# Performance work log

Hardware: AMD Instinct MI355X
Metric: run time of the kernel (lower is better)

Reference implementation:

```python
import jax, jax.numpy as jnp
import numpy as np

B, S, L, F, CD, NH, E, HID = 4, 1024, 256, 512, 768, 8, 8, 2048


def _xavier(k, shape):
    std = float(np.sqrt(1.0 / (shape[-2] + shape[-1])))
    return jax.random.normal(k, shape, dtype=jnp.float32) * std


def setup_inputs() -> dict:
    key = jax.random.key(0)
    ks = iter(jax.random.split(key, 64))
    nk = lambda: next(ks)
    inp = {}
    inp['x_r'] = jax.random.normal(nk(), (B, S, F), jnp.float32)
    inp['x_i'] = jax.random.normal(nk(), (B, S, F), jnp.float32)
    inp['ctx_r'] = jax.random.normal(nk(), (B, L, CD), jnp.float32)
    inp['ctx_i'] = jax.random.normal(nk(), (B, L, CD), jnp.float32)
    inp['ln1_g'] = jnp.ones((F,), jnp.float32)
    inp['ln2_g'] = jnp.ones((F,), jnp.float32)
    inp['ln3_g'] = jnp.ones((F,), jnp.float32)
    for pref, shp in [('sa_q', (F, F)), ('sa_k', (F, F)), ('sa_v', (F, F)), ('sa_o', (F, F)),
                      ('ca_q', (F, F)), ('ca_k', (CD, F)), ('ca_v', (CD, F)), ('ca_o', (F, F))]:
        inp[pref + 'Wr'] = _xavier(nk(), shp)
        inp[pref + 'Wi'] = _xavier(nk(), shp)
        inp[pref + 'br'] = jnp.zeros((F,), jnp.float32)
        inp[pref + 'bi'] = jnp.zeros((F,), jnp.float32)
    inp['moe_W1r'] = _xavier(nk(), (E, F, HID))
    inp['moe_W1i'] = _xavier(nk(), (E, F, HID))
    inp['moe_b1r'] = jnp.zeros((E, HID), jnp.float32)
    inp['moe_b1i'] = jnp.zeros((E, HID), jnp.float32)
    inp['moe_mb'] = jnp.zeros((E, HID), jnp.float32)  # modReLU bias
    inp['moe_W2r'] = _xavier(nk(), (E, HID, F))
    inp['moe_W2i'] = _xavier(nk(), (E, HID, F))
    inp['moe_b2r'] = jnp.zeros((E, F), jnp.float32)
    inp['moe_b2i'] = jnp.zeros((E, F), jnp.float32)
    return inp


def _clin(xr, xi, Wr, Wi, br, bi):
    # (xr + i xi) @ (Wr + i Wi) + (br + i bi)
    return xr @ Wr - xi @ Wi + br, xr @ Wi + xi @ Wr + bi


def _cln(xr, xi, g, eps=1e-6):
    amp = jnp.sqrt(xr * xr + xi * xi + eps)
    s = g * (amp / (jnp.mean(amp, axis=-1, keepdims=True) + eps)) / (amp + eps)
    return xr * s, xi * s


def _modrelu(xr, xi, b, eps=1e-10):
    amp = jnp.sqrt(xr * xr + xi * xi + eps)
    s = jax.nn.relu(amp + b) / (amp + eps)
    return xr * s, xi * s


def _cattn(xr, xi, cr, ci, qWr, qWi, qbr, qbi, kWr, kWi, kbr, kbi,
           vWr, vWi, vbr, vbi, oWr, oWi, obr, obi, nh):
    qr, qi = _clin(xr, xi, qWr, qWi, qbr, qbi)
    kr, ki = _clin(cr, ci, kWr, kWi, kbr, kbi)
    vr, vi = _clin(cr, ci, vWr, vWi, vbr, vbi)
    Bt, Sq, Ft = qr.shape
    Sk = kr.shape[1]
    d = Ft // nh
    sp = lambda t: t.reshape(Bt, t.shape[1], nh, d).transpose(0, 2, 1, 3)  # b n s d
    Qr, Qi, Kr, Ki, Vr, Vi = sp(qr), sp(qi), sp(kr), sp(ki), sp(vr), sp(vi)
    scale = 1.0 / float(d) ** 0.5
    scores = (jnp.einsum('bnqd,bnkd->bnqk', Qr, Kr)
              + jnp.einsum('bnqd,bnkd->bnqk', Qi, Ki)) * scale
    w = jax.nn.softmax(scores, axis=-1)
    mix = lambda t: jnp.einsum('bnqk,bnkd->bnqd', w, t).transpose(0, 2, 1, 3).reshape(Bt, Sq, Ft)
    return _clin(mix(Vr), mix(Vi), oWr, oWi, obr, obi)


def reference(x_r, x_i, ctx_r, ctx_i, ln1_g, ln2_g, ln3_g,
              sa_qWr, sa_qWi, sa_qbr, sa_qbi, sa_kWr, sa_kWi, sa_kbr, sa_kbi,
              sa_vWr, sa_vWi, sa_vbr, sa_vbi, sa_oWr, sa_oWi, sa_obr, sa_obi,
              ca_qWr, ca_qWi, ca_qbr, ca_qbi, ca_kWr, ca_kWi, ca_kbr, ca_kbi,
              ca_vWr, ca_vWi, ca_vbr, ca_vbi, ca_oWr, ca_oWi, ca_obr, ca_obi,
              moe_W1r, moe_W1i, moe_b1r, moe_b1i, moe_mb,
              moe_W2r, moe_W2i, moe_b2r, moe_b2i):
    # self-attention block
    hr, hi = _cln(x_r, x_i, ln1_g)
    ar, ai = _cattn(hr, hi, hr, hi, sa_qWr, sa_qWi, sa_qbr, sa_qbi,
                    sa_kWr, sa_kWi, sa_kbr, sa_kbi, sa_vWr, sa_vWi, sa_vbr, sa_vbi,
                    sa_oWr, sa_oWi, sa_obr, sa_obi, NH)
    xr, xi = x_r + ar, x_i + ai
    # cross-attention block
    hr, hi = _cln(xr, xi, ln2_g)
    ar, ai = _cattn(hr, hi, ctx_r, ctx_i, ca_qWr, ca_qWi, ca_qbr, ca_qbi,
                    ca_kWr, ca_kWi, ca_kbr, ca_kbi, ca_vWr, ca_vWi, ca_vbr, ca_vbi,
                    ca_oWr, ca_oWi, ca_obr, ca_obi, NH)
    xr, xi = xr + ar, xi + ai
    # phase-routed MoE block
    hr, hi = _cln(xr, xi, ln3_g)
    phase = jnp.arctan2(hi, hr)
    token_phase = jnp.arctan2(jnp.mean(jnp.sin(phase), axis=-1),
                              jnp.mean(jnp.cos(phase), axis=-1))
    idx = jnp.clip(jnp.floor((token_phase + jnp.pi) / (2.0 * jnp.pi) * E).astype(jnp.int32), 0, E - 1)
    acc_r = jnp.zeros_like(hr)
    acc_i = jnp.zeros_like(hi)
    for e in range(E):  # dense-compute-then-mask, faithful to source
        ur, ui = _clin(hr, hi, moe_W1r[e], moe_W1i[e], moe_b1r[e], moe_b1i[e])
        ur, ui = _modrelu(ur, ui, moe_mb[e])
        yr, yi = _clin(ur, ui, moe_W2r[e], moe_W2i[e], moe_b2r[e], moe_b2i[e])
        m = (idx == e).astype(hr.dtype)[..., None]
        acc_r = acc_r + yr * m
        acc_i = acc_i + yi * m
    xr, xi = xr + acc_r, xi + acc_i
    return jnp.stack([xr, xi])  # [2, B, S, F] real/imag
```

## Files before the change

kernel.cpp:

```cpp
#include <hip/hip_runtime.h>
#include <hip/hip_bf16.h>
#include <math.h>


#define NTOK 4096
#define FF   512
#define CDIM 768
#define NEXP 8
#define HID  2048
#define TMAX128 40
#define NPAD128 (TMAX128 * 128)

typedef __hip_bfloat16 bf16;
typedef short bf16x8 __attribute__((ext_vector_type(8)));
typedef float f32x4  __attribute__((ext_vector_type(4)));

struct Ptr6 { const float* p[6]; };
struct WPackAll {
    const float* sR[8]; const float* sI[8];
    bf16* dR[8]; bf16* dI[8];
    int kdiv[8];
};

__device__ __forceinline__ short f2bf(float x) {
// ... 129 lines not shown
    for (int j = 0; j < 8; j++) {
        float a = sR[(long)(kb + j) * N + n];
        bf16 ah = __float2bfloat16(a);
        dR[dbase + j] = lo ? __float2bfloat16(a - __bfloat162float(ah)) : ah;
        float b = sI[(long)(kb + j) * N + n];
        bf16 bh = __float2bfloat16(b);
        dI[dbase + j] = lo ? __float2bfloat16(b - __bfloat162float(bh)) : bh;
    }
}

__global__ __launch_bounds__(256)
void convW_packed(const float* __restrict__ sR, const float* __restrict__ sI,
                  bf16* __restrict__ dR, bf16* __restrict__ dI,
                  int N, long estride)
{
    int g = blockIdx.x * 256 + threadIdx.x;
    int nt = g >> 6, l = g & 63;
    int kc = blockIdx.y;
    int e  = blockIdx.z;
    const float* srcR = sR + (long)e * estride;
    const float* srcI = sI + (long)e * estride;
    bf16* dstR = dR + (long)e * estride;
    bf16* dstI = dI + (long)e * estride;
    int kb = kc * 32 + (l >> 4) * 8;
    int n  = nt * 16 + (l & 15);
    long dbase = ((long)kc * (N >> 4) + nt) * 512 + l * 8;
#pragma unroll
    for (int j = 0; j < 8; j++) {
        dstR[dbase + j] = __float2bfloat16(srcR[(long)(kb + j) * N + n]);
        dstI[dbase + j] = __float2bfloat16(srcI[(long)(kb + j) * N + n]);
    }
}

template<bool X3, bool EXPERT, bool GATHER, bool MODRELU, bool OUTBF16>
__global__ __launch_bounds__(256, 2)
void cgemm128(const bf16* __restrict__ Ar, const bf16* __restrict__ Ai,
              int lda, int Kreal,
              const bf16* __restrict__ Wr0, const bf16* __restrict__ Wi0,
              long wz, long westride, int ntTot, int kdiv,
              Ptr6 bias, int bstride, const float* __restrict__ mb,
              void* __restrict__ Cr0, void* __restrict__ Ci0, long cz,
              int ldc, int Kp, int bandM,
              const int* __restrict__ order, const int* __restrict__ tileExpert)
{
    __shared__ short sA[16384];
    __shared__ short sW[16384];
    int tm, tn, z;
    if (bandM > 0) {
        int L = blockIdx.x;
        int xcd = L & 7, idx = L >> 3;
        tm = xcd * bandM + idx % bandM;
        tn = idx / bandM;
        z = 0;
    } else {
        tm = blockIdx.x; tn = blockIdx.y; z = blockIdx.z;
    }
    const bf16* Wr = Wr0 + (long)z * wz;
    const bf16* Wi = Wi0 + (long)z * wz;
    const float* br = bias.p[2 * z];
    const float* bi = bias.p[2 * z + 1];
    void* Crv = (char*)Cr0 + (long)z * cz;
    void* Civ = (char*)Ci0 + (long)z * cz;
    if (EXPERT) {
        int e = tileExpert[tm];
        if (e < 0) return;
        Wr += (long)e * westride;  Wi += (long)e * westride;
        br += (long)e * bstride;   bi += (long)e * bstride;
        if (MODRELU) mb += (long)e * bstride;
    }
    int t = threadIdx.x;
    int l = t & 63, w = t >> 6;
    int riS = w >> 1, kcS = w & 1;
    const bf16* Asrc = riS ? Ai : Ar;
// ... 34 lines not shown
        for (int ntl = 0; ntl < 8; ntl++)
            gload16(wb + (ntl << 9),
                    &sW[(((riS * 2 + kcS) * 8 + ntl) << 9)]);
        __syncthreads();
#pragma unroll
        for (int kc = 0; kc < 2; kc++) {
            bf16x8 wrf[4], wif[4];
#pragma unroll
            for (int sn = 0; sn < 4; sn++) {
                wrf[sn] = *(const bf16x8*)&sW[(((kc * 8) + wn * 4 + sn) << 9) + l * 8];
                wif[sn] = *(const bf16x8*)&sW[((((2 + kc) * 8) + wn * 4 + sn) << 9) + l * 8];
            }
#pragma unroll
            for (int sm = 0; sm < 4; sm++) {
                bf16x8 ar = *(const bf16x8*)&sA[(((kc * 8) + wm * 4 + sm) << 9) + l * 8];
                bf16x8 ai = *(const bf16x8*)&sA[((((2 + kc) * 8) + wm * 4 + sm) << 9) + l * 8];
                bf16x8 na = ai ^ sgn;
#pragma unroll
                for (int sn = 0; sn < 4; sn++) {
                    accR[sm][sn] = __builtin_amdgcn_mfma_f32_16x16x32_bf16(ar, wrf[sn], accR[sm][sn], 0, 0, 0);
                    accR[sm][sn] = __builtin_amdgcn_mfma_f32_16x16x32_bf16(na, wif[sn], accR[sm][sn], 0, 0, 0);
                    accI[sm][sn] = __builtin_amdgcn_mfma_f32_16x16x32_bf16(ar, wif[sn], accI[sm][sn], 0, 0, 0);
                    accI[sm][sn] = __builtin_amdgcn_mfma_f32_16x16x32_bf16(ai, wrf[sn], accI[sm][sn], 0, 0, 0);
                }
            }
        }
    }
#pragma unroll
    for (int sm = 0; sm < 4; sm++)
#pragma unroll
        for (int sn = 0; sn < 4; sn++) {
            int row0 = tm * 128 + wm * 64 + sm * 16 + (l >> 4) * 4;
            int col  = tn * 128 + wn * 64 + sn * 16 + (l & 15);
            float bre = br[col], bie = bi[col];
            float mbe = MODRELU ? mb[col] : 0.f;
#pragma unroll
            for (int v = 0; v < 4; v++) {
                int row = row0 + v;
                float vr = accR[sm][sn][v] + bre;
                float vi = accI[sm][sn][v] + bie;
                if (MODRELU) {
                    float amp = sqrtf(vr * vr + vi * vi + 1e-10f);
                    float sc = fmaxf(amp + mbe, 0.f) / (amp + 1e-10f);
                    vr *= sc; vi *= sc;
                }
                long cidx = (long)row * ldc + col;
                if (OUTBF16) {
                    ((bf16*)Crv)[cidx] = __float2bfloat16(vr);
                    ((bf16*)Civ)[cidx] = __float2bfloat16(vi);
                } else {
                    ((float*)Crv)[cidx] = vr;
                    ((float*)Civ)[cidx] = vi;
                }
            }
        }
}

template<bool X3, bool EXPERT, bool GATHER, bool MODRELU, bool RESID, bool OUTBF16>
__global__ __launch_bounds__(256)
void cgemm_mfma(const bf16* __restrict__ Ar, const bf16* __restrict__ Ai,
                int lda, int Kreal,
                const bf16* __restrict__ Wr0, const bf16* __restrict__ Wi0,
                long wz, long westride, int ntTot, int kdiv,
                Ptr6 bias, int bstride, const float* __restrict__ mb,
                const float* __restrict__ Rr, const float* __restrict__ Ri,
                void* __restrict__ Cr0, void* __restrict__ Ci0, long cz,
                int ldc, int Kp,
                const int* __restrict__ order, const int* __restrict__ tileExpert)
{
    __shared__ short sA[8192];
    __shared__ short sW[8192];
    int tm = blockIdx.x, tn = blockIdx.y, z = blockIdx.z;
    const bf16* Wr = Wr0 + (long)z * wz;
    const bf16* Wi = Wi0 + (long)z * wz;
    const float* br = bias.p[2 * z];
    const float* bi = bias.p[2 * z + 1];
    void* Crv = (char*)Cr0 + (long)z * cz;
    void* Civ = (char*)Ci0 + (long)z * cz;
    if (EXPERT) {
        int e = tileExpert[tm];
        if (e < 0) return;
        Wr += (long)e * westride;  Wi += (long)e * westride;
        br += (long)e * bstride;   bi += (long)e * bstride;
        if (MODRELU) mb += (long)e * bstride;
    }
    int t = threadIdx.x;
    int l = t & 63, jj = t >> 6;
    int riS = jj >> 1, kcS = jj & 1;
    const bf16* Asrc = riS ? Ai : Ar;
    const bf16* Wsrc = riS ? Wi : Wr;
    int kq8 = (l >> 4) * 8;
    long arb[4];
#pragma unroll
    for (int mt = 0; mt < 4; mt++) {
        int grow = tm * 64 + mt * 16 + (l & 15);
        int tok = grow;
        if (GATHER) { int gg = order[grow]; tok = (gg < 0) ? 0 : gg; }
        arb[mt] = (long)tok * lda;
    }
    int wm = jj & 1, wn = jj >> 1;

    f32x4 zf = {0.f, 0.f, 0.f, 0.f};
    f32x4 accR[2][2], accI[2][2];
#pragma unroll
    for (int a = 0; a < 2; a++)
#pragma unroll
        for (int b = 0; b < 2; b++) { accR[a][b] = zf; accI[a][b] = zf; }

    const bf16x8 sgn = {(short)0x8000,(short)0x8000,(short)0x8000,(short)0x8000,
                        (short)0x8000,(short)0x8000,(short)0x8000,(short)0x8000};

    for (int k0 = 0; k0 < Kp; k0 += 64) {
        __syncthreads();
        int lc = k0 + kcS * 32;
        int acol = (X3 && lc >= 2 * Kreal) ? lc - 2 * Kreal : lc;
#pragma unroll
        for (int mt = 0; mt < 4; mt++)
            gload16(Asrc + arb[mt] + acol + kq8,
                    &sA[(((riS * 2 + kcS) << 2) + mt) << 9]);
        int kcl = (k0 >> 5) + kcS;
        int pkc = (X3 && kcl >= kdiv) ? kcl - kdiv : kcl;
        const bf16* wbase = Wsrc + (((long)pkc * ntTot + tn * 4) << 9) + l * 8;
#pragma unroll
        for (int ntl = 0; ntl < 4; ntl++)
            gload16(wbase + (ntl << 9),
                    &sW[(((riS * 2 + kcS) << 2) + ntl) << 9]);
        __syncthreads();
#pragma unroll
        for (int kc = 0; kc < 2; kc++) {
            bf16x8 arf[2], aif[2], naf[2], wrf[2], wif[2];
#pragma unroll
            for (int s = 0; s < 2; s++) {
                arf[s] = *(const bf16x8*)&sA[(((kc << 2) + wm * 2 + s) << 9) + l * 8];
                aif[s] = *(const bf16x8*)&sA[((((2 + kc) << 2) + wm * 2 + s) << 9) + l * 8];
                naf[s] = aif[s] ^ sgn;
                wrf[s] = *(const bf16x8*)&sW[(((kc << 2) + wn * 2 + s) << 9) + l * 8];
                wif[s] = *(const bf16x8*)&sW[((((2 + kc) << 2) + wn * 2 + s) << 9) + l * 8];
            }
#pragma unroll
            for (int sm = 0; sm < 2; sm++)
#pragma unroll
                for (int sn = 0; sn < 2; sn++) {
                    accR[sm][sn] = __builtin_amdgcn_mfma_f32_16x16x32_bf16(arf[sm], wrf[sn], accR[sm][sn], 0, 0, 0);
                    accR[sm][sn] = __builtin_amdgcn_mfma_f32_16x16x32_bf16(naf[sm], wif[sn], accR[sm][sn], 0, 0, 0);
                    accI[sm][sn] = __builtin_amdgcn_mfma_f32_16x16x32_bf16(arf[sm], wif[sn], accI[sm][sn], 0, 0, 0);
                    accI[sm][sn] = __builtin_amdgcn_mfma_f32_16x16x32_bf16(aif[sm], wrf[sn], accI[sm][sn], 0, 0, 0);
                }
        }
    }
#pragma unroll
    for (int sm = 0; sm < 2; sm++)
#pragma unroll
        for (int sn = 0; sn < 2; sn++) {
            int row0 = tm * 64 + (wm * 2 + sm) * 16 + (l >> 4) * 4;
            int col  = tn * 64 + (wn * 2 + sn) * 16 + (l & 15);
            float bre = br[col], bie = bi[col];
            float mbe = MODRELU ? mb[col] : 0.f;
#pragma unroll
            for (int v = 0; v < 4; v++) {
                int row = row0 + v;
                float vr = accR[sm][sn][v] + bre;
                float vi = accI[sm][sn][v] + bie;
                if (MODRELU) {
                    float amp = sqrtf(vr * vr + vi * vi + 1e-10f);
                    float sc = fmaxf(amp + mbe, 0.f) / (amp + 1e-10f);
                    vr *= sc; vi *= sc;
                }
                long cidx = (long)row * ldc + col;
                if (RESID) { vr += Rr[cidx]; vi += Ri[cidx]; }
                if (OUTBF16) {
                    ((bf16*)Crv)[cidx] = __float2bfloat16(vr);
                    ((bf16*)Civ)[cidx] = __float2bfloat16(vi);
                } else {
                    ((float*)Crv)[cidx] = vr;
                    ((float*)Civ)[cidx] = vi;
                }
            }
        }
}

__global__ __launch_bounds__(256)
void pack_kv(const float* __restrict__ kr, const float* __restrict__ ki,
             const float* __restrict__ vr, const float* __restrict__ vi,
             short* __restrict__ pK, short* __restrict__ pV, int Sk)
{
    const int F = FF;
    int kt = blockIdx.x, h = blockIdx.y, b = blockIdx.z;
    int nkt = gridDim.x;
    long blkbase = ((long)((b * 8 + h) * nkt) + kt) * 8192;
    int t = threadIdx.x;
#pragma unroll
    for (int it = 0; it < 2; it++) {
        int s = t + 256 * it;
        int sl = s & 63, g = s >> 6;
        int ri = g >> 2, c = (g >> 1) & 1, nt = g & 1;
        int sq = sl >> 4, sn = sl & 15;
        const float* src = ri ? ki : kr;
        long base = ((long)(b * Sk + kt * 32 + nt * 16 + sn)) * F + h * 64 + c * 32 + sq * 8;
        long outH = blkbase + ((((ri * 2 + 0) * 2 + c) * 2 + nt) * 64 + sl) * 8;
        long outL = blkbase + ((((ri * 2 + 1) * 2 + c) * 2 + nt) * 64 + sl) * 8;
#pragma unroll
        for (int j = 0; j < 8; j++) {
            float x = src[base + j];
            short xh = f2bf(x);
            pK[outH + j] = xh;
            pK[outL + j] = f2bf(x - bf2f(xh));
        }
    }
#pragma unroll
    for (int it = 0; it < 2; it++) {
        int s = t + 256 * it;
        int sl = s & 63, g = s >> 6;
        int ri = g >> 2, nt = g & 3;
        int sq = sl >> 4, sn = sl & 15;
        const float* src = ri ? vi : vr;
        long base = ((long)(b * Sk + kt * 32 + sq * 8)) * F + h * 64 + nt * 16 + sn;
        long outH = blkbase + (((ri * 2 + 0) * 4 + nt) * 64 + sl) * 8;
        long outL = blkbase + (((ri * 2 + 1) * 4 + nt) * 64 + sl) * 8;
#pragma unroll
        for (int j = 0; j < 8; j++) {
            float x = src[base + (long)j * F];
            short xh = f2bf(x);
            pV[outH + j] = xh;
            pV[outL + j] = f2bf(x - bf2f(xh));
        }
    }
}

__global__ __launch_bounds__(256)
void cattn_mfma(const float* __restrict__ qr, const float* __restrict__ qi,
                const short* __restrict__ pK, const short* __restrict__ pV,
                bf16* __restrict__ dR, bf16* __restrict__ dI,
                int S, int Sk)
{
    __shared__ short sK[8192];
    __shared__ short sV[8192];
    __shared__ short sP[5120];
    const int F = FF;
    int L = blockIdx.x;
    int xcd = L & 7, idx = L >> 3;
    int bh = xcd * 4 + (idx & 3);
    int qt = idx >> 2;
    int b = bh >> 3, h = bh & 7;
    int t = threadIdx.x;
    int w = t >> 6, l = t & 63, q = l >> 4, n16 = l & 15;

    bf16x8 qh_[2][2], ql_[2][2];
    {
        long qbase = ((long)(b * S + qt * 64 + w * 16 + n16)) * F + h * 64 + q * 8;
#pragma unroll
        for (int ri = 0; ri < 2; ri++) {
            const float* src = ri ? qi : qr;
#pragma unroll
            for (int c = 0; c < 2; c++) {
                float vv[8];
                *(float4*)&vv[0] = *(const float4*)&src[qbase + c * 32];
                *(float4*)&vv[4] = *(const float4*)&src[qbase + c * 32 + 4];
#pragma unroll
                for (int j = 0; j < 8; j++) {
                    short xh = f2bf(vv[j]);
                    qh_[ri][c][j] = xh;
                    ql_[ri][c][j] = f2bf(vv[j] - bf2f(xh));
                }
            }
        }
    }

    f32x4 zf = {0.f, 0.f, 0.f, 0.f};
    f32x4 oR[4], oI[4];
#pragma unroll
    for (int nt = 0; nt < 4; nt++) { oR[nt] = zf; oI[nt] = zf; }
    float m_run[4] = {-3.0e38f, -3.0e38f, -3.0e38f, -3.0e38f};
    float l_run[4] = {0.f, 0.f, 0.f, 0.f};

    int nkt = Sk >> 5;
    long pbh = (long)((b * 8 + h) * nkt) * 8192;
    for (int kt = 0; kt < nkt; kt++) {
        __syncthreads();
        long pb = pbh + (long)kt * 8192;
#pragma unroll
        for (int i = 0; i < 4; i++) {
            int bk = w * 4 + i;
            gload16(pK + pb + (bk << 9) + l * 8, &sK[bk << 9]);
            gload16(pV + pb + (bk << 9) + l * 8, &sV[bk << 9]);
        }
        __syncthreads();

        f32x4 sc[2];
        sc[0] = zf; sc[1] = zf;
#pragma unroll
        for (int nt = 0; nt < 2; nt++) {
#pragma unroll
            for (int ri = 0; ri < 2; ri++) {
                bf16x8 kh0 = *(const bf16x8*)&sK[((((ri * 2 + 0) * 2 + 0) * 2 + nt) * 64 + l) * 8];
                bf16x8 kh1 = *(const bf16x8*)&sK[((((ri * 2 + 0) * 2 + 1) * 2 + nt) * 64 + l) * 8];
                bf16x8 kl0 = *(const bf16x8*)&sK[((((ri * 2 + 1) * 2 + 0) * 2 + nt) * 64 + l) * 8];
                bf16x8 kl1 = *(const bf16x8*)&sK[((((ri * 2 + 1) * 2 + 1) * 2 + nt) * 64 + l) * 8];
                sc[nt] = __builtin_amdgcn_mfma_f32_16x16x32_bf16(qh_[ri][0], kh0, sc[nt], 0, 0, 0);
                sc[nt] = __builtin_amdgcn_mfma_f32_16x16x32_bf16(qh_[ri][1], kh1, sc[nt], 0, 0, 0);
                sc[nt] = __builtin_amdgcn_mfma_f32_16x16x32_bf16(ql_[ri][0], kh0, sc[nt], 0, 0, 0);
                sc[nt] = __builtin_amdgcn_mfma_f32_16x16x32_bf16(ql_[ri][1], kh1, sc[nt], 0, 0, 0);
                sc[nt] = __builtin_amdgcn_mfma_f32_16x16x32_bf16(qh_[ri][0], kl0, sc[nt], 0, 0, 0);
                sc[nt] = __builtin_amdgcn_mfma_f32_16x16x32_bf16(qh_[ri][1], kl1, sc[nt], 0, 0, 0);
            }
        }
        float alpha[4];
#pragma unroll
        for (int v = 0; v < 4; v++) {
            float s0 = sc[0][v] * 0.125f, s1 = sc[1][v] * 0.125f;
            float mx = fmaxf(s0, s1);
            mx = fmaxf(mx, __shfl_xor(mx, 1));
            mx = fmaxf(mx, __shfl_xor(mx, 2));
            mx = fmaxf(mx, __shfl_xor(mx, 4));
            mx = fmaxf(mx, __shfl_xor(mx, 8));
            float mnew = fmaxf(m_run[v], mx);
            float p0 = __expf(s0 - mnew), p1 = __expf(s1 - mnew);
            sc[0][v] = p0; sc[1][v] = p1;
            float ps = p0 + p1;
            ps += __shfl_xor(ps, 1);
            ps += __shfl_xor(ps, 2);
            ps += __shfl_xor(ps, 4);
            ps += __shfl_xor(ps, 8);
            alpha[v] = __expf(m_run[v] - mnew);
            l_run[v] = l_run[v] * alpha[v] + ps;
            m_run[v] = mnew;
        }
#pragma unroll
        for (int nt = 0; nt < 4; nt++)
#pragma unroll
            for (int v = 0; v < 4; v++) { oR[nt][v] *= alpha[v]; oI[nt][v] *= alpha[v]; }
        int pbase = w * 1280;
#pragma unroll
        for (int nt = 0; nt < 2; nt++)
#pragma unroll
            for (int v = 0; v < 4; v++) {
                float p = sc[nt][v];
                short ph = f2bf(p);
                short pl = f2bf(p - bf2f(ph));
                int idxp = pbase + (q * 4 + v) * 40 + nt * 16 + n16;
                sP[idxp] = ph;
                sP[idxp + 640] = pl;
            }
        bf16x8 pH = *(const bf16x8*)&sP[pbase + n16 * 40 + q * 8];
        bf16x8 pL = *(const bf16x8*)&sP[pbase + 640 + n16 * 40 + q * 8];
#pragma unroll
        for (int nt = 0; nt < 4; nt++) {
            bf16x8 vh = *(const bf16x8*)&sV[(((0 * 2 + 0) * 4 + nt) * 64 + l) * 8];
            bf16x8 vl = *(const bf16x8*)&sV[(((0 * 2 + 1) * 4 + nt) * 64 + l) * 8];
            oR[nt] = __builtin_amdgcn_mfma_f32_16x16x32_bf16(pH, vh, oR[nt], 0, 0, 0);
            oR[nt] = __builtin_amdgcn_mfma_f32_16x16x32_bf16(pL, vh, oR[nt], 0, 0, 0);
            oR[nt] = __builtin_amdgcn_mfma_f32_16x16x32_bf16(pH, vl, oR[nt], 0, 0, 0);
            bf16x8 wh = *(const bf16x8*)&sV[(((1 * 2 + 0) * 4 + nt) * 64 + l) * 8];
            bf16x8 wl2 = *(const bf16x8*)&sV[(((1 * 2 + 1) * 4 + nt) * 64 + l) * 8];
            oI[nt] = __builtin_amdgcn_mfma_f32_16x16x32_bf16(pH, wh, oI[nt], 0, 0, 0);
            oI[nt] = __builtin_amdgcn_mfma_f32_16x16x32_bf16(pL, wh, oI[nt], 0, 0, 0);
            oI[nt] = __builtin_amdgcn_mfma_f32_16x16x32_bf16(pH, wl2, oI[nt], 0, 0, 0);
        }
    }
#pragma unroll
    for (int v = 0; v < 4; v++) {
        float inv = 1.0f / l_run[v];
        long rbase = ((long)(b * S + qt * 64 + w * 16 + q * 4 + v)) * 1024;
#pragma unroll
        for (int nt = 0; nt < 4; nt++) {
            int col = h * 64 + nt * 16 + n16;
            float vr = oR[nt][v] * inv;
            bf16 hh = __float2bfloat16(vr);
            dR[rbase + col] = hh;
            dR[rbase + 512 + col] = __float2bfloat16(vr - __bfloat162float(hh));
            float vi = oI[nt][v] * inv;
            bf16 hi2 = __float2bfloat16(vi);
            dI[rbase + col] = hi2;
            dI[rbase + 512 + col] = __float2bfloat16(vi - __bfloat162float(hi2));
        }
    }
}

__global__ __launch_bounds__(256)
void moe_build_kernel(const int* __restrict__ eidx, int* __restrict__ order,
                      int* __restrict__ te128, int* __restrict__ te64)
{
    __shared__ int cnt[NEXP], segbase[NEXP], cursor[NEXP], tb128[NEXP], n128[NEXP];
    int t = threadIdx.x;
    if (t < NEXP) { cnt[t] = 0; cursor[t] = 0; }
    __syncthreads();
    for (int i = t; i < NTOK; i += 256) atomicAdd(&cnt[eidx[i]], 1);
    __syncthreads();
    if (t == 0) {
        int ob = 0, tb = 0;
// ... 120 lines not shown
    bf16* cak_r = saq_r + 12 * PS1;              bf16* cak_i = cak_r + PS2;
    bf16* cav_r = cak_r + 2 * PS2;               bf16* cav_i = cak_r + 3 * PS2;
    bf16* Wm_r = (bf16*)Q;
    bf16* Wm_i = (bf16*)(Q + 16777216);
    char* ints = W + 12 * NF4 + 41943040 + 524288;
    int* eidx  = (int*)ints;
    int* order = eidx + NTOK;
    int* te128 = order + NPAD128;
    int* te64  = te128 + 64;

    dim3 blk(256);
    const long W1S = (long)FF * HID;
    const long CZ = 2 * NF4;
    Ptr6 bQKV = {{sa_qbr, sa_qbi, sa_kbr, sa_kbi, sa_vbr, sa_vbi}};
    Ptr6 bSAO = {{sa_obr, sa_obi, 0, 0, 0, 0}};
    Ptr6 bCAQ = {{ca_qbr, ca_qbi, 0, 0, 0, 0}};
    Ptr6 bCKV = {{ca_kbr, ca_kbi, ca_vbr, ca_vbi, 0, 0}};
    Ptr6 bCAO = {{ca_obr, ca_obi, 0, 0, 0, 0}};
    Ptr6 bM1  = {{moe_b1r, moe_b1i, 0, 0, 0, 0}};
    Ptr6 bM2  = {{moe_b2r, moe_b2i, 0, 0, 0, 0}};

    WPackAll wp;
    wp.sR[0]=sa_qWr; wp.sI[0]=sa_qWi; wp.dR[0]=saq_r; wp.dI[0]=saq_i; wp.kdiv[0]=16;
    wp.sR[1]=sa_kWr; wp.sI[1]=sa_kWi; wp.dR[1]=sak_r; wp.dI[1]=sak_i; wp.kdiv[1]=16;
    wp.sR[2]=sa_vWr; wp.sI[2]=sa_vWi; wp.dR[2]=sav_r; wp.dI[2]=sav_i; wp.kdiv[2]=16;
    wp.sR[3]=sa_oWr; wp.sI[3]=sa_oWi; wp.dR[3]=sao_r; wp.dI[3]=sao_i; wp.kdiv[3]=16;
    wp.sR[4]=ca_qWr; wp.sI[4]=ca_qWi; wp.dR[4]=caq_r; wp.dI[4]=caq_i; wp.kdiv[4]=16;
    wp.sR[5]=ca_oWr; wp.sI[5]=ca_oWi; wp.dR[5]=cao_r; wp.dI[5]=cao_i; wp.kdiv[5]=16;
    wp.sR[6]=ca_kWr; wp.sI[6]=ca_kWi; wp.dR[6]=cak_r; wp.dI[6]=cak_i; wp.kdiv[6]=24;
    wp.sR[7]=ca_vWr; wp.sI[7]=ca_vWi; wp.dR[7]=cav_r; wp.dI[7]=cav_i; wp.kdiv[7]=24;
    expandW_all<<<dim3(8, 48, 8), blk, 0, stream>>>(wp);

    cln_expand<<<NTOK, blk, 0, stream>>>(x_r, x_i, ln1_g, A1r, A1i);
    cgemm128<true,false,false,false,false><<<dim3(32, 4, 3), blk, 0, stream>>>(
        A1r, A1i, 1024, 512, saq_r, saq_i, 2 * PS1, 0, 32, 16,
        bQKV, 0, nullptr, qr, qi, CZ, FF, 1536, 0, nullptr, nullptr);
    pack_kv<<<dim3(32, 8, 4), blk, 0, stream>>>(kr, ki, vr, vi, pKbuf, pVbuf, 1024);
    cattn_mfma<<<512, blk, 0, stream>>>(qr, qi, pKbuf, pVbuf, A1r, A1i, 1024, 1024);
    cgemm_mfma<true,false,false,false,true,false><<<dim3(64, 8, 1), blk, 0, stream>>>(
        A1r, A1i, 1024, 512, sao_r, sao_i, 0, 0, 32, 16,
        bSAO, 0, nullptr, x_r, x_i, xr, xi, 0, FF, 1536, nullptr, nullptr);

    cln_expand<<<NTOK, blk, 0, stream>>>(xr, xi, ln2_g, A1r, A1i);
    cgemm_mfma<true,false,false,false,false,false><<<dim3(64, 8, 1), blk, 0, stream>>>(
        A1r, A1i, 1024, 512, caq_r, caq_i, 0, 0, 32, 16,
        bCAQ, 0, nullptr, nullptr, nullptr, qr, qi, 0, FF, 1536, nullptr, nullptr);
    expandA_x2<<<dim3(3, 1024), blk, 0, stream>>>(ctx_r, ctx_i, A2r, A2i, CDIM);
    cgemm_mfma<true,false,false,false,false,false><<<dim3(16, 8, 2), blk, 0, stream>>>(
        A2r, A2i, 1536, 768, cak_r, cak_i, 2 * PS2, 0, 32, 24,
        bCKV, 0, nullptr, nullptr, nullptr, kr, ki, CZ, FF, 2304, nullptr, nullptr);
    pack_kv<<<dim3(8, 8, 4), blk, 0, stream>>>(kr, ki, vr, vi, pKbuf, pVbuf, 256);
    cattn_mfma<<<512, blk, 0, stream>>>(qr, qi, pKbuf, pVbuf, A1r, A1i, 1024, 256);
    cgemm_mfma<true,false,false,false,true,false><<<dim3(64, 8, 1), blk, 0, stream>>>(
        A1r, A1i, 1024, 512, cao_r, cao_i, 0, 0, 32, 16,
        bCAO, 0, nullptr, xr, xi, xr, xi, 0, FF, 1536, nullptr, nullptr);

    cln_route<<<NTOK, blk, 0, stream>>>(xr, xi, ln3_g, h3r, h3i, eidx);
    moe_build_kernel<<<1, blk, 0, stream>>>(eidx, order, te128, te64);
    convW_packed<<<dim3(32, 16, 8), blk, 0, stream>>>(moe_W1r, moe_W1i, Wm_r, Wm_i, HID, W1S);
    cgemm128<false,true,true,true,true><<<640, blk, 0, stream>>>(
        h3r, h3i, 512, 512, Wm_r, Wm_i, 0, W1S, 128, 0,
        bM1, HID, moe_mb, u_r, u_i, 0, HID, 512, 5, order, te128);
    convW_packed<<<dim3(8, 64, 8), blk, 0, stream>>>(moe_W2r, moe_W2i, Wm_r, Wm_i, FF, W1S);
    cgemm128<false,true,false,false,false><<<160, blk, 0, stream>>>(
        u_r, u_i, 2048, 2048, Wm_r, Wm_i, 0, W1S, 32, 0,
        bM2, FF, nullptr, y_r, y_i, 0, FF, 2048, 5, nullptr, te128);
    combine_kernel<<<NPAD128, blk, 0, stream>>>(order, xr, xi, y_r, y_i, out);
}
```

Measured before the change: 866.4 us.

## Double attention key tile to 64 and move projection GEMMs to 128-tile kernel

The attention kernel now processes 64 keys per iteration instead of 32. K/V packing, shared buffers and the P-staging are resized to match, and P now reuses the sK buffer behind an extra barrier. The 4096x512 projection GEMMs (self-attn output, cross-attn Q and output) switch from the 64x64-tile kernel to the 128x128-tile kernel with XCD banding, and that kernel gains a residual-add epilogue. The aim is to halve per-key-tile loop and barrier overhead and to improve data reuse, at the cost of more LDS per block and fewer blocks (128) for the projection GEMMs.

```diff
diff --git a/kernel.cpp b/kernel.cpp
--- a/kernel.cpp
+++ b/kernel.cpp
@@ -185,13 +185,14 @@
     }
 }
 
-template<bool X3, bool EXPERT, bool GATHER, bool MODRELU, bool OUTBF16>
+template<bool X3, bool EXPERT, bool GATHER, bool MODRELU, bool RESID, bool OUTBF16>
 __global__ __launch_bounds__(256, 2)
 void cgemm128(const bf16* __restrict__ Ar, const bf16* __restrict__ Ai,
               int lda, int Kreal,
               const bf16* __restrict__ Wr0, const bf16* __restrict__ Wi0,
               long wz, long westride, int ntTot, int kdiv,
               Ptr6 bias, int bstride, const float* __restrict__ mb,
+              const float* __restrict__ Rr, const float* __restrict__ Ri,
               void* __restrict__ Cr0, void* __restrict__ Ci0, long cz,
               int ldc, int Kp, int bandM,
               const int* __restrict__ order, const int* __restrict__ tileExpert)
@@ -292,128 +293,6 @@
         for (int sn = 0; sn < 4; sn++) {
             int row0 = tm * 128 + wm * 64 + sm * 16 + (l >> 4) * 4;
             int col  = tn * 128 + wn * 64 + sn * 16 + (l & 15);
-            float bre = br[col], bie = bi[col];
-            float mbe = MODRELU ? mb[col] : 0.f;
-#pragma unroll
-            for (int v = 0; v < 4; v++) {
-                int row = row0 + v;
-                float vr = accR[sm][sn][v] + bre;
-                float vi = accI[sm][sn][v] + bie;
-                if (MODRELU) {
-                    float amp = sqrtf(vr * vr + vi * vi + 1e-10f);
-                    float sc = fmaxf(amp + mbe, 0.f) / (amp + 1e-10f);
-                    vr *= sc; vi *= sc;
-                }
-                long cidx = (long)row * ldc + col;
-                if (OUTBF16) {
-                    ((bf16*)Crv)[cidx] = __float2bfloat16(vr);
-                    ((bf16*)Civ)[cidx] = __float2bfloat16(vi);
-                } else {
-                    ((float*)Crv)[cidx] = vr;
-                    ((float*)Civ)[cidx] = vi;
-                }
-            }
-        }
-}
-
-template<bool X3, bool EXPERT, bool GATHER, bool MODRELU, bool RESID, bool OUTBF16>
-__global__ __launch_bounds__(256)
-void cgemm_mfma(const bf16* __restrict__ Ar, const bf16* __restrict__ Ai,
-                int lda, int Kreal,
-                const bf16* __restrict__ Wr0, const bf16* __restrict__ Wi0,
-                long wz, long westride, int ntTot, int kdiv,
-                Ptr6 bias, int bstride, const float* __restrict__ mb,
-                const float* __restrict__ Rr, const float* __restrict__ Ri,
-                void* __restrict__ Cr0, void* __restrict__ Ci0, long cz,
-                int ldc, int Kp,
-                const int* __restrict__ order, const int* __restrict__ tileExpert)
-{
-    __shared__ short sA[8192];
-    __shared__ short sW[8192];
-    int tm = blockIdx.x, tn = blockIdx.y, z = blockIdx.z;
-    const bf16* Wr = Wr0 + (long)z * wz;
-    const bf16* Wi = Wi0 + (long)z * wz;
-    const float* br = bias.p[2 * z];
-    const float* bi = bias.p[2 * z + 1];
-    void* Crv = (char*)Cr0 + (long)z * cz;
-    void* Civ = (char*)Ci0 + (long)z * cz;
-    if (EXPERT) {
-        int e = tileExpert[tm];
-        if (e < 0) return;
-        Wr += (long)e * westride;  Wi += (long)e * westride;
-        br += (long)e * bstride;   bi += (long)e * bstride;
-        if (MODRELU) mb += (long)e * bstride;
-    }
-    int t = threadIdx.x;
-    int l = t & 63, jj = t >> 6;
-    int riS = jj >> 1, kcS = jj & 1;
-    const bf16* Asrc = riS ? Ai : Ar;
-    const bf16* Wsrc = riS ? Wi : Wr;
-    int kq8 = (l >> 4) * 8;
-    long arb[4];
-#pragma unroll
-    for (int mt = 0; mt < 4; mt++) {
-        int grow = tm * 64 + mt * 16 + (l & 15);
-        int tok = grow;
-        if (GATHER) { int gg = order[grow]; tok = (gg < 0) ? 0 : gg; }
-        arb[mt] = (long)tok * lda;
-    }
-    int wm = jj & 1, wn = jj >> 1;
-
-    f32x4 zf = {0.f, 0.f, 0.f, 0.f};
-    f32x4 accR[2][2], accI[2][2];
-#pragma unroll
-    for (int a = 0; a < 2; a++)
-#pragma unroll
-        for (int b = 0; b < 2; b++) { accR[a][b] = zf; accI[a][b] = zf; }
-
-    const bf16x8 sgn = {(short)0x8000,(short)0x8000,(short)0x8000,(short)0x8000,
-                        (short)0x8000,(short)0x8000,(short)0x8000,(short)0x8000};
-
-    for (int k0 = 0; k0 < Kp; k0 += 64) {
-        __syncthreads();
-        int lc = k0 + kcS * 32;
-        int acol = (X3 && lc >= 2 * Kreal) ? lc - 2 * Kreal : lc;
-#pragma unroll
-        for (int mt = 0; mt < 4; mt++)
-            gload16(Asrc + arb[mt] + acol + kq8,
-                    &sA[(((riS * 2 + kcS) << 2) + mt) << 9]);
-        int kcl = (k0 >> 5) + kcS;
-        int pkc = (X3 && kcl >= kdiv) ? kcl - kdiv : kcl;
-        const bf16* wbase = Wsrc + (((long)pkc * ntTot + tn * 4) << 9) + l * 8;
-#pragma unroll
-        for (int ntl = 0; ntl < 4; ntl++)
-            gload16(wbase + (ntl << 9),
-                    &sW[(((riS * 2 + kcS) << 2) + ntl) << 9]);
-        __syncthreads();
-#pragma unroll
-        for (int kc = 0; kc < 2; kc++) {
-            bf16x8 arf[2], aif[2], naf[2], wrf[2], wif[2];
-#pragma unroll
-            for (int s = 0; s < 2; s++) {
-                arf[s] = *(const bf16x8*)&sA[(((kc << 2) + wm * 2 + s) << 9) + l * 8];
-                aif[s] = *(const bf16x8*)&sA[((((2 + kc) << 2) + wm * 2 + s) << 9) + l * 8];
-                naf[s] = aif[s] ^ sgn;
-                wrf[s] = *(const bf16x8*)&sW[(((kc << 2) + wn * 2 + s) << 9) + l * 8];
-                wif[s] = *(const bf16x8*)&sW[((((2 + kc) << 2) + wn * 2 + s) << 9) + l * 8];
-            }
-#pragma unroll
-            for (int sm = 0; sm < 2; sm++)
-#pragma unroll
-                for (int sn = 0; sn < 2; sn++) {
-                    accR[sm][sn] = __builtin_amdgcn_mfma_f32_16x16x32_bf16(arf[sm], wrf[sn], accR[sm][sn], 0, 0, 0);
-                    accR[sm][sn] = __builtin_amdgcn_mfma_f32_16x16x32_bf16(naf[sm], wif[sn], accR[sm][sn], 0, 0, 0);
-                    accI[sm][sn] = __builtin_amdgcn_mfma_f32_16x16x32_bf16(arf[sm], wif[sn], accI[sm][sn], 0, 0, 0);
-                    accI[sm][sn] = __builtin_amdgcn_mfma_f32_16x16x32_bf16(aif[sm], wrf[sn], accI[sm][sn], 0, 0, 0);
-                }
-        }
-    }
-#pragma unroll
-    for (int sm = 0; sm < 2; sm++)
-#pragma unroll
-        for (int sn = 0; sn < 2; sn++) {
-            int row0 = tm * 64 + (wm * 2 + sm) * 16 + (l >> 4) * 4;
-            int col  = tn * 64 + (wn * 2 + sn) * 16 + (l & 15);
             float bre = br[col], bie = bi[col];
             float mbe = MODRELU ? mb[col] : 0.f;
 #pragma unroll
@@ -439,6 +318,129 @@
         }
 }
 
+template<bool X3, bool EXPERT, bool GATHER, bool MODRELU, bool RESID, bool OUTBF16>
+__global__ __launch_bounds__(256)
+void cgemm_mfma(const bf16* __restrict__ Ar, const bf16* __restrict__ Ai,
+                int lda, int Kreal,
+                const bf16* __restrict__ Wr0, const bf16* __restrict__ Wi0,
+                long wz, long westride, int ntTot, int kdiv,
+                Ptr6 bias, int bstride, const float* __restrict__ mb,
+                const float* __restrict__ Rr, const float* __restrict__ Ri,
+                void* __restrict__ Cr0, void* __restrict__ Ci0, long cz,
+                int ldc, int Kp,
+                const int* __restrict__ order, const int* __restrict__ tileExpert)
+{
+    __shared__ short sA[8192];
+    __shared__ short sW[8192];
+    int tm = blockIdx.x, tn = blockIdx.y, z = blockIdx.z;
+    const bf16* Wr = Wr0 + (long)z * wz;
+    const bf16* Wi = Wi0 + (long)z * wz;
+    const float* br = bias.p[2 * z];
+    const float* bi = bias.p[2 * z + 1];
+    void* Crv = (char*)Cr0 + (long)z * cz;
+    void* Civ = (char*)Ci0 + (long)z * cz;
+    if (EXPERT) {
+        int e = tileExpert[tm];
+        if (e < 0) return;
+        Wr += (long)e * westride;  Wi += (long)e * westride;
+        br += (long)e * bstride;   bi += (long)e * bstride;
+        if (MODRELU) mb += (long)e * bstride;
+    }
+    int t = threadIdx.x;
+    int l = t & 63, jj = t >> 6;
+    int riS = jj >> 1, kcS = jj & 1;
+    const bf16* Asrc = riS ? Ai : Ar;
+    const bf16* Wsrc = riS ? Wi : Wr;
+    int kq8 = (l >> 4) * 8;
+    long arb[4];
+#pragma unroll
+    for (int mt = 0; mt < 4; mt++) {
+        int grow = tm * 64 + mt * 16 + (l & 15);
+        int tok = grow;
+        if (GATHER) { int gg = order[grow]; tok = (gg < 0) ? 0 : gg; }
+        arb[mt] = (long)tok * lda;
+    }
+    int wm = jj & 1, wn = jj >> 1;
+
+    f32x4 zf = {0.f, 0.f, 0.f, 0.f};
+    f32x4 accR[2][2], accI[2][2];
+#pragma unroll
+    for (int a = 0; a < 2; a++)
+#pragma unroll
+        for (int b = 0; b < 2; b++) { accR[a][b] = zf; accI[a][b] = zf; }
+
+    const bf16x8 sgn = {(short)0x8000,(short)0x8000,(short)0x8000,(short)0x8000,
+                        (short)0x8000,(short)0x8000,(short)0x8000,(short)0x8000};
+
+    for (int k0 = 0; k0 < Kp; k0 += 64) {
+        __syncthreads();
+        int lc = k0 + kcS * 32;
+        int acol = (X3 && lc >= 2 * Kreal) ? lc - 2 * Kreal : lc;
+#pragma unroll
+        for (int mt = 0; mt < 4; mt++)
+            gload16(Asrc + arb[mt] + acol + kq8,
+                    &sA[(((riS * 2 + kcS) << 2) + mt) << 9]);
+        int kcl = (k0 >> 5) + kcS;
+        int pkc = (X3 && kcl >= kdiv) ? kcl - kdiv : kcl;
+        const bf16* wbase = Wsrc + (((long)pkc * ntTot + tn * 4) << 9) + l * 8;
+#pragma unroll
+        for (int ntl = 0; ntl < 4; ntl++)
+            gload16(wbase + (ntl << 9),
+                    &sW[(((riS * 2 + kcS) << 2) + ntl) << 9]);
+        __syncthreads();
+#pragma unroll
+        for (int kc = 0; kc < 2; kc++) {
+            bf16x8 arf[2], aif[2], naf[2], wrf[2], wif[2];
+#pragma unroll
+            for (int s = 0; s < 2; s++) {
+                arf[s] = *(const bf16x8*)&sA[(((kc << 2) + wm * 2 + s) << 9) + l * 8];
+                aif[s] = *(const bf16x8*)&sA[((((2 + kc) << 2) + wm * 2 + s) << 9) + l * 8];
+                naf[s] = aif[s] ^ sgn;
+                wrf[s] = *(const bf16x8*)&sW[(((kc << 2) + wn * 2 + s) << 9) + l * 8];
+                wif[s] = *(const bf16x8*)&sW[((((2 + kc) << 2) + wn * 2 + s) << 9) + l * 8];
+            }
+#pragma unroll
+            for (int sm = 0; sm < 2; sm++)
+#pragma unroll
+                for (int sn = 0; sn < 2; sn++) {
+                    accR[sm][sn] = __builtin_amdgcn_mfma_f32_16x16x32_bf16(arf[sm], wrf[sn], accR[sm][sn], 0, 0, 0);
+                    accR[sm][sn] = __builtin_amdgcn_mfma_f32_16x16x32_bf16(naf[sm], wif[sn], accR[sm][sn], 0, 0, 0);
+                    accI[sm][sn] = __builtin_amdgcn_mfma_f32_16x16x32_bf16(arf[sm], wif[sn], accI[sm][sn], 0, 0, 0);
+                    accI[sm][sn] = __builtin_amdgcn_mfma_f32_16x16x32_bf16(aif[sm], wrf[sn], accI[sm][sn], 0, 0, 0);
+                }
+        }
+    }
+#pragma unroll
+    for (int sm = 0; sm < 2; sm++)
+#pragma unroll
+        for (int sn = 0; sn < 2; sn++) {
+            int row0 = tm * 64 + (wm * 2 + sm) * 16 + (l >> 4) * 4;
+            int col  = tn * 64 + (wn * 2 + sn) * 16 + (l & 15);
+            float bre = br[col], bie = bi[col];
+            float mbe = MODRELU ? mb[col] : 0.f;
+#pragma unroll
+            for (int v = 0; v < 4; v++) {
+                int row = row0 + v;
+                float vr = accR[sm][sn][v] + bre;
+                float vi = accI[sm][sn][v] + bie;
+                if (MODRELU) {
+                    float amp = sqrtf(vr * vr + vi * vi + 1e-10f);
+                    float sc = fmaxf(amp + mbe, 0.f) / (amp + 1e-10f);
+                    vr *= sc; vi *= sc;
+                }
+                long cidx = (long)row * ldc + col;
+                if (RESID) { vr += Rr[cidx]; vi += Ri[cidx]; }
+                if (OUTBF16) {
+                    ((bf16*)Crv)[cidx] = __float2bfloat16(vr);
+                    ((bf16*)Civ)[cidx] = __float2bfloat16(vi);
+                } else {
+                    ((float*)Crv)[cidx] = vr;
+                    ((float*)Civ)[cidx] = vi;
+                }
+            }
+        }
+}
+
 __global__ __launch_bounds__(256)
 void pack_kv(const float* __restrict__ kr, const float* __restrict__ ki,
              const float* __restrict__ vr, const float* __restrict__ vi,
@@ -447,18 +449,18 @@
     const int F = FF;
     int kt = blockIdx.x, h = blockIdx.y, b = blockIdx.z;
     int nkt = gridDim.x;
-    long blkbase = ((long)((b * 8 + h) * nkt) + kt) * 8192;
+    long blkbase = ((long)((b * 8 + h) * nkt) + kt) * 16384;
     int t = threadIdx.x;
 #pragma unroll
-    for (int it = 0; it < 2; it++) {
-        int s = t + 256 * it;
-        int sl = s & 63, g = s >> 6;
-        int ri = g >> 2, c = (g >> 1) & 1, nt = g & 1;
+    for (int it = 0; it < 4; it++) {
+        int p4 = t + 256 * it;
+        int sl = p4 & 63, gg = p4 >> 6;
+        int nt = gg & 3, c = (gg >> 2) & 1, ri = gg >> 3;
         int sq = sl >> 4, sn = sl & 15;
         const float* src = ri ? ki : kr;
-        long base = ((long)(b * Sk + kt * 32 + nt * 16 + sn)) * F + h * 64 + c * 32 + sq * 8;
-        long outH = blkbase + ((((ri * 2 + 0) * 2 + c) * 2 + nt) * 64 + sl) * 8;
-        long outL = blkbase + ((((ri * 2 + 1) * 2 + c) * 2 + nt) * 64 + sl) * 8;
+        long base = ((long)(b * Sk + kt * 64 + nt * 16 + sn)) * F + h * 64 + c * 32 + sq * 8;
+        long outH = blkbase + ((((ri * 2 + 0) * 2 + c) * 4 + nt) * 64 + sl) * 8;
+        long outL = blkbase + ((((ri * 2 + 1) * 2 + c) * 4 + nt) * 64 + sl) * 8;
 #pragma unroll
         for (int j = 0; j < 8; j++) {
             float x = src[base + j];
@@ -468,15 +470,15 @@
         }
     }
 #pragma unroll
-    for (int it = 0; it < 2; it++) {
-        int s = t + 256 * it;
-        int sl = s & 63, g = s >> 6;
-        int ri = g >> 2, nt = g & 3;
+    for (int it = 0; it < 4; it++) {
+        int p4 = t + 256 * it;
+        int sl = p4 & 63, gg = p4 >> 6;
+        int nt = gg & 3, kc = (gg >> 2) & 1, ri = gg >> 3;
         int sq = sl >> 4, sn = sl & 15;
         const float* src = ri ? vi : vr;
-        long base = ((long)(b * Sk + kt * 32 + sq * 8)) * F + h * 64 + nt * 16 + sn;
-        long outH = blkbase + (((ri * 2 + 0) * 4 + nt) * 64 + sl) * 8;
-        long outL = blkbase + (((ri * 2 + 1) * 4 + nt) * 64 + sl) * 8;
+        long base = ((long)(b * Sk + kt * 64 + kc * 32 + sq * 8)) * F + h * 64 + nt * 16 + sn;
+        long outH = blkbase + ((((ri * 2 + 0) * 2 + kc) * 4 + nt) * 64 + sl) * 8;
+        long outL = blkbase + ((((ri * 2 + 1) * 2 + kc) * 4 + nt) * 64 + sl) * 8;
 #pragma unroll
         for (int j = 0; j < 8; j++) {
             float x = src[base + (long)j * F];
@@ -493,9 +495,8 @@
                 bf16* __restrict__ dR, bf16* __restrict__ dI,
                 int S, int Sk)
 {
-    __shared__ short sK[8192];
-    __shared__ short sV[8192];
-    __shared__ short sP[5120];
+    __shared__ short sK[16384];
+    __shared__ short sV[16384];
     const int F = FF;
     int L = blockIdx.x;
     int xcd = L & 7, idx = L >> 3;
@@ -533,29 +534,29 @@
     float m_run[4] = {-3.0e38f, -3.0e38f, -3.0e38f, -3.0e38f};
     float l_run[4] = {0.f, 0.f, 0.f, 0.f};
 
-    int nkt = Sk >> 5;
-    long pbh = (long)((b * 8 + h) * nkt) * 8192;
+    int nkt = Sk >> 6;
+    long pbh = (long)((b * 8 + h) * nkt) * 16384;
     for (int kt = 0; kt < nkt; kt++) {
         __syncthreads();
-        long pb = pbh + (long)kt * 8192;
-#pragma unroll
-        for (int i = 0; i < 4; i++) {
-            int bk = w * 4 + i;
+        long pb = pbh + (long)kt * 16384;
+#pragma unroll
+        for (int i = 0; i < 8; i++) {
+            int bk = w * 8 + i;
             gload16(pK + pb + (bk << 9) + l * 8, &sK[bk << 9]);
             gload16(pV + pb + (bk << 9) + l * 8, &sV[bk << 9]);
         }
         __syncthreads();
 
-        f32x4 sc[2];
-        sc[0] = zf; sc[1] = zf;
-#pragma unroll
-        for (int nt = 0; nt < 2; nt++) {
+        f32x4 sc[4];
+        sc[0] = zf; sc[1] = zf; sc[2] = zf; sc[3] = zf;
+#pragma unroll
+        for (int nt = 0; nt < 4; nt++) {
 #pragma unroll
             for (int ri = 0; ri < 2; ri++) {
-                bf16x8 kh0 = *(const bf16x8*)&sK[((((ri * 2 + 0) * 2 + 0) * 2 + nt) * 64 + l) * 8];
-                bf16x8 kh1 = *(const bf16x8*)&sK[((((ri * 2 + 0) * 2 + 1) * 2 + nt) * 64 + l) * 8];
-                bf16x8 kl0 = *(const bf16x8*)&sK[((((ri * 2 + 1) * 2 + 0) * 2 + nt) * 64 + l) * 8];
-                bf16x8 kl1 = *(const bf16x8*)&sK[((((ri * 2 + 1) * 2 + 1) * 2 + nt) * 64 + l) * 8];
+                bf16x8 kh0 = *(const bf16x8*)&sK[((((ri * 2 + 0) * 2 + 0) * 4 + nt) * 64 + l) * 8];
+                bf16x8 kh1 = *(const bf16x8*)&sK[((((ri * 2 + 0) * 2 + 1) * 4 + nt) * 64 + l) * 8];
+                bf16x8 kl0 = *(const bf16x8*)&sK[((((ri * 2 + 1) * 2 + 0) * 4 + nt) * 64 + l) * 8];
+                bf16x8 kl1 = *(const bf16x8*)&sK[((((ri * 2 + 1) * 2 + 1) * 4 + nt) * 64 + l) * 8];
                 sc[nt] = __builtin_amdgcn_mfma_f32_16x16x32_bf16(qh_[ri][0], kh0, sc[nt], 0, 0, 0);
                 sc[nt] = __builtin_amdgcn_mfma_f32_16x16x32_bf16(qh_[ri][1], kh1, sc[nt], 0, 0, 0);
                 sc[nt] = __builtin_amdgcn_mfma_f32_16x16x32_bf16(ql_[ri][0], kh0, sc[nt], 0, 0, 0);
@@ -568,15 +569,17 @@
 #pragma unroll
         for (int v = 0; v < 4; v++) {
             float s0 = sc[0][v] * 0.125f, s1 = sc[1][v] * 0.125f;
-            float mx = fmaxf(s0, s1);
+            float s2 = sc[2][v] * 0.125f, s3 = sc[3][v] * 0.125f;
+            float mx = fmaxf(fmaxf(s0, s1), fmaxf(s2, s3));
             mx = fmaxf(mx, __shfl_xor(mx, 1));
             mx = fmaxf(mx, __shfl_xor(mx, 2));
             mx = fmaxf(mx, __shfl_xor(mx, 4));
             mx = fmaxf(mx, __shfl_xor(mx, 8));
             float mnew = fmaxf(m_run[v], mx);
             float p0 = __expf(s0 - mnew), p1 = __expf(s1 - mnew);
-            sc[0][v] = p0; sc[1][v] = p1;
-            float ps = p0 + p1;
+            float p2 = __expf(s2 - mnew), p3 = __expf(s3 - mnew);
+            sc[0][v] = p0; sc[1][v] = p1; sc[2][v] = p2; sc[3][v] = p3;
+            float ps = (p0 + p1) + (p2 + p3);
             ps += __shfl_xor(ps, 1);
             ps += __shfl_xor(ps, 2);
             ps += __shfl_xor(ps, 4);
@@ -589,32 +592,43 @@
         for (int nt = 0; nt < 4; nt++)
 #pragma unroll
             for (int v = 0; v < 4; v++) { oR[nt][v] *= alpha[v]; oI[nt][v] *= alpha[v]; }
-        int pbase = w * 1280;
-#pragma unroll
-        for (int nt = 0; nt < 2; nt++)
+        __syncthreads();
+        int pbase = w * 2560;
+#pragma unroll
+        for (int nt = 0; nt < 4; nt++) {
+            int kc = nt >> 1;
+            int kk = (nt & 1) * 16 + n16;
 #pragma unroll
             for (int v = 0; v < 4; v++) {
                 float p = sc[nt][v];
                 short ph = f2bf(p);
                 short pl = f2bf(p - bf2f(ph));
-                int idxp = pbase + (q * 4 + v) * 40 + nt * 16 + n16;
-                sP[idxp] = ph;
-                sP[idxp + 640] = pl;
+                int idxp = pbase + kc * 640 + (q * 4 + v) * 40 + kk;
+                sK[idxp] = ph;
+                sK[idxp + 1280] = pl;
             }
-        bf16x8 pH = *(const bf16x8*)&sP[pbase + n16 * 40 + q * 8];
-        bf16x8 pL = *(const bf16x8*)&sP[pbase + 640 + n16 * 40 + q * 8];
+        }
+        bf16x8 pH[2], pL[2];
+#pragma unroll
+        for (int kc = 0; kc < 2; kc++) {
+            pH[kc] = *(const bf16x8*)&sK[pbase + kc * 640 + n16 * 40 + q * 8];
+            pL[kc] = *(const bf16x8*)&sK[pbase + 1280 + kc * 640 + n16 * 40 + q * 8];
+        }
 #pragma unroll
         for (int nt = 0; nt < 4; nt++) {
-            bf16x8 vh = *(const bf16x8*)&sV[(((0 * 2 + 0) * 4 + nt) * 64 + l) * 8];
-            bf16x8 vl = *(const bf16x8*)&sV[(((0 * 2 + 1) * 4 + nt) * 64 + l) * 8];
-            oR[nt] = __builtin_amdgcn_mfma_f32_16x16x32_bf16(pH, vh, oR[nt], 0, 0, 0);
-            oR[nt] = __builtin_amdgcn_mfma_f32_16x16x32_bf16(pL, vh, oR[nt], 0, 0, 0);
-            oR[nt] = __builtin_amdgcn_mfma_f32_16x16x32_bf16(pH, vl, oR[nt], 0, 0, 0);
-            bf16x8 wh = *(const bf16x8*)&sV[(((1 * 2 + 0) * 4 + nt) * 64 + l) * 8];
-            bf16x8 wl2 = *(const bf16x8*)&sV[(((1 * 2 + 1) * 4 + nt) * 64 + l) * 8];
-            oI[nt] = __builtin_amdgcn_mfma_f32_16x16x32_bf16(pH, wh, oI[nt], 0, 0, 0);
-            oI[nt] = __builtin_amdgcn_mfma_f32_16x16x32_bf16(pL, wh, oI[nt], 0, 0, 0);
-            oI[nt] = __builtin_amdgcn_mfma_f32_16x16x32_bf16(pH, wl2, oI[nt], 0, 0, 0);
+#pragma unroll
+            for (int kc = 0; kc < 2; kc++) {
+                bf16x8 vh  = *(const bf16x8*)&sV[((((0 * 2 + 0) * 2 + kc) * 4 + nt) * 64 + l) * 8];
+                bf16x8 vl  = *(const bf16x8*)&sV[((((0 * 2 + 1) * 2 + kc) * 4 + nt) * 64 + l) * 8];
+                oR[nt] = __builtin_amdgcn_mfma_f32_16x16x32_bf16(pH[kc], vh, oR[nt], 0, 0, 0);
+                oR[nt] = __builtin_amdgcn_mfma_f32_16x16x32_bf16(pL[kc], vh, oR[nt], 0, 0, 0);
+                oR[nt] = __builtin_amdgcn_mfma_f32_16x16x32_bf16(pH[kc], vl, oR[nt], 0, 0, 0);
+                bf16x8 wh  = *(const bf16x8*)&sV[((((1 * 2 + 0) * 2 + kc) * 4 + nt) * 64 + l) * 8];
+                bf16x8 wl2 = *(const bf16x8*)&sV[((((1 * 2 + 1) * 2 + kc) * 4 + nt) * 64 + l) * 8];
+                oI[nt] = __builtin_amdgcn_mfma_f32_16x16x32_bf16(pH[kc], wh, oI[nt], 0, 0, 0);
+                oI[nt] = __builtin_amdgcn_mfma_f32_16x16x32_bf16(pL[kc], wh, oI[nt], 0, 0, 0);
+                oI[nt] = __builtin_amdgcn_mfma_f32_16x16x32_bf16(pH[kc], wl2, oI[nt], 0, 0, 0);
+            }
         }
     }
 #pragma unroll
@@ -801,38 +815,38 @@
     expandW_all<<<dim3(8, 48, 8), blk, 0, stream>>>(wp);
 
     cln_expand<<<NTOK, blk, 0, stream>>>(x_r, x_i, ln1_g, A1r, A1i);
-    cgemm128<true,false,false,false,false><<<dim3(32, 4, 3), blk, 0, stream>>>(
+    cgemm128<true,false,false,false,false,false><<<dim3(32, 4, 3), blk, 0, stream>>>(
         A1r, A1i, 1024, 512, saq_r, saq_i, 2 * PS1, 0, 32, 16,
-        bQKV, 0, nullptr, qr, qi, CZ, FF, 1536, 0, nullptr, nullptr);
-    pack_kv<<<dim3(32, 8, 4), blk, 0, stream>>>(kr, ki, vr, vi, pKbuf, pVbuf, 1024);
+        bQKV, 0, nullptr, nullptr, nullptr, qr, qi, CZ, FF, 1536, 0, nullptr, nullptr);
+    pack_kv<<<dim3(16, 8, 4), blk, 0, stream>>>(kr, ki, vr, vi, pKbuf, pVbuf, 1024);
     cattn_mfma<<<512, blk, 0, stream>>>(qr, qi, pKbuf, pVbuf, A1r, A1i, 1024, 1024);
-    cgemm_mfma<true,false,false,false,true,false><<<dim3(64, 8, 1), blk, 0, stream>>>(
+    cgemm128<true,false,false,false,true,false><<<128, blk, 0, stream>>>(
         A1r, A1i, 1024, 512, sao_r, sao_i, 0, 0, 32, 16,
-        bSAO, 0, nullptr, x_r, x_i, xr, xi, 0, FF, 1536, nullptr, nullptr);
+        bSAO, 0, nullptr, x_r, x_i, xr, xi, 0, FF, 1536, 4, nullptr, nullptr);
 
     cln_expand<<<NTOK, blk, 0, stream>>>(xr, xi, ln2_g, A1r, A1i);
-    cgemm_mfma<true,false,false,false,false,false><<<dim3(64, 8, 1), blk, 0, stream>>>(
+    cgemm128<true,false,false,false,false,false><<<128, blk, 0, stream>>>(
         A1r, A1i, 1024, 512, caq_r, caq_i, 0, 0, 32, 16,
-        bCAQ, 0, nullptr, nullptr, nullptr, qr, qi, 0, FF, 1536, nullptr, nullptr);
+        bCAQ, 0, nullptr, nullptr, nullptr, qr, qi, 0, FF, 1536, 4, nullptr, nullptr);
     expandA_x2<<<dim3(3, 1024), blk, 0, stream>>>(ctx_r, ctx_i, A2r, A2i, CDIM);
     cgemm_mfma<true,false,false,false,false,false><<<dim3(16, 8, 2), blk, 0, stream>>>(
         A2r, A2i, 1536, 768, cak_r, cak_i, 2 * PS2, 0, 32, 24,
         bCKV, 0, nullptr, nullptr, nullptr, kr, ki, CZ, FF, 2304, nullptr, nullptr);
-    pack_kv<<<dim3(8, 8, 4), blk, 0, stream>>>(kr, ki, vr, vi, pKbuf, pVbuf, 256);
+    pack_kv<<<dim3(4, 8, 4), blk, 0, stream>>>(kr, ki, vr, vi, pKbuf, pVbuf, 256);
     cattn_mfma<<<512, blk, 0, stream>>>(qr, qi, pKbuf, pVbuf, A1r, A1i, 1024, 256);
-    cgemm_mfma<true,false,false,false,true,false><<<dim3(64, 8, 1), blk, 0, stream>>>(
+    cgemm128<true,false,false,false,true,false><<<128, blk, 0, stream>>>(
         A1r, A1i, 1024, 512, cao_r, cao_i, 0, 0, 32, 16,
-        bCAO, 0, nullptr, xr, xi, xr, xi, 0, FF, 1536, nullptr, nullptr);
+        bCAO, 0, nullptr, xr, xi, xr, xi, 0, FF, 1536, 4, nullptr, nullptr);
 
     cln_route<<<NTOK, blk, 0, stream>>>(xr, xi, ln3_g, h3r, h3i, eidx);
     moe_build_kernel<<<1, blk, 0, stream>>>(eidx, order, te128, te64);
     convW_packed<<<dim3(32, 16, 8), blk, 0, stream>>>(moe_W1r, moe_W1i, Wm_r, Wm_i, HID, W1S);
-    cgemm128<false,true,true,true,true><<<640, blk, 0, stream>>>(
+    cgemm128<false,true,true,true,false,true><<<640, blk, 0, stream>>>(
         h3r, h3i, 512, 512, Wm_r, Wm_i, 0, W1S, 128, 0,
-        bM1, HID, moe_mb, u_r, u_i, 0, HID, 512, 5, order, te128);
+        bM1, HID, moe_mb, nullptr, nullptr, u_r, u_i, 0, HID, 512, 5, order, te128);
     convW_packed<<<dim3(8, 64, 8), blk, 0, stream>>>(moe_W2r, moe_W2i, Wm_r, Wm_i, FF, W1S);
-    cgemm128<false,true,false,false,false><<<160, blk, 0, stream>>>(
+    cgemm128<false,true,false,false,false,false><<<160, blk, 0, stream>>>(
         u_r, u_i, 2048, 2048, Wm_r, Wm_i, 0, W1S, 32, 0,
-        bM2, FF, nullptr, y_r, y_i, 0, FF, 2048, 5, nullptr, te128);
+        bM2, FF, nullptr, nullptr, nullptr, y_r, y_i, 0, FF, 2048, 5, nullptr, te128);
     combine_kernel<<<NPAD128, blk, 0, stream>>>(order, xr, xi, y_r, y_i, out);
 }
```

New measurement: 948.3 us. 9.4% more time.
